# Optimization experiments

Measured on AMD Instinct MI355X. Metric: run time of the kernel, lower is better.

The kernel has to match this reference:

```python
import jax, jax.numpy as jnp
import numpy as np
from jax import lax

B, L = 2048, 2048
CIN, CONV, D, NCLS = 1, 128, 1024, 1000
E, H, K = 6, 2 * 1024, 2  # num_experts, expert hidden, top-k


def setup_inputs() -> dict:
    key = jax.random.key(0)
    ks = jax.random.split(key, 16)
    s = lambda *sh: 0.02
    return {
        "x": jax.random.normal(ks[0], (B, L), jnp.float32),
        "conv1_w": jax.random.normal(ks[1], (CONV, CIN, 5), jnp.float32) * 0.1,
        "conv1_b": jnp.zeros((CONV,), jnp.float32),
        "conv2_w": jax.random.normal(ks[2], (CONV, CONV, 5), jnp.float32) * 0.05,
        "conv2_b": jnp.zeros((CONV,), jnp.float32),
        "proj_w": jax.random.normal(ks[3], (D, CONV), jnp.float32) * 0.05,
        "proj_b": jnp.zeros((D,), jnp.float32),
        "router_w": jax.random.normal(ks[4], (E, D), jnp.float32) * 0.02,
        "router_b": jnp.zeros((E,), jnp.float32),
        "exp_w1": jax.random.normal(ks[5], (E, H, D), jnp.float32) * 0.02,
        "exp_b1": jnp.zeros((E, H), jnp.float32),
        "exp_w2": jax.random.normal(ks[6], (E, D, H), jnp.float32) * 0.02,
        "exp_b2": jnp.zeros((E, D), jnp.float32),
        "cls_w": jax.random.normal(ks[7], (NCLS, D), jnp.float32) * 0.02,
        "cls_b": jnp.zeros((NCLS,), jnp.float32),
    }


def _conv1d(x, w, b):
    # x: [B, C, L]; torch Conv1d(k=5, stride=2, pad=2)
    y = lax.conv_general_dilated(x, w, window_strides=(2,), padding=[(2, 2)],
                                 dimension_numbers=("NCH", "OIH", "NCH"))
    return y + b[None, :, None]


def reference(x, conv1_w, conv1_b, conv2_w, conv2_b, proj_w, proj_b,
              router_w, router_b, exp_w1, exp_b1, exp_w2, exp_b2, cls_w, cls_b):
    h = x[:, None, :]                               # [B,1,L]
    h = jax.nn.relu(_conv1d(h, conv1_w, conv1_b))   # [B,CONV,L/2]
    h = jax.nn.relu(_conv1d(h, conv2_w, conv2_b))   # [B,CONV,L/4]
    h = h.mean(axis=-1)                             # [B,CONV]
    h = h @ proj_w.T + proj_b                       # [B,D]

    # Top-2 router
    probs = jax.nn.softmax(h @ router_w.T + router_b, axis=-1)  # [B,E]
    top_vals, top_idx = lax.top_k(probs, K)                     # [B,2]
    # per-token per-expert combine weights (exact same math as masked loop)
    combine = (jax.nn.one_hot(top_idx[:, 0], E, dtype=h.dtype) * top_vals[:, 0:1]
               + jax.nn.one_hot(top_idx[:, 1], E, dtype=h.dtype) * top_vals[:, 1:2])  # [B,E]

    # all-expert FFN, then masked combine (equivalent to gather/scatter dispatch)
    hid = jax.nn.relu(jnp.einsum("bd,ehd->beh", h, exp_w1) + exp_b1)  # [B,E,H]
    eo = jnp.einsum("beh,edh->bed", hid, exp_w2) + exp_b2             # [B,E,D]
    moe = jnp.einsum("be,bed->bd", combine, eo)                       # [B,D]

    return moe @ cls_w.T + cls_b                                      # [B,NCLS]
```

## Files before the change

### kernel.cpp

```cpp
#include <hip/hip_runtime.h>
#include <hip/hip_bf16.h>
#include <hip/hip_fp16.h>
#include <stdint.h>

#define BB 2048
#define LL 2048
#define CV 128
#define DD 1024
#define NC 1000
#define EE 6
#define HH 2048

typedef __bf16 bf16_t;
typedef _Float16 f16_t;
typedef __attribute__((ext_vector_type(8))) __bf16 bf16x8;
typedef __attribute__((ext_vector_type(4))) __bf16 bf16x4;
typedef __attribute__((ext_vector_type(8))) _Float16 f16x8;
typedef __attribute__((ext_vector_type(4))) _Float16 f16x4;
typedef __attribute__((ext_vector_type(4))) float f32x4;

__global__ void k_prep_w2(const float* __restrict__ w2, bf16_t* __restrict__ wsw)
{
    int idx = blockIdx.x * 256 + threadIdx.x;
    if (idx >= 5 * 128 * 128) return;
    int kk = idx % 5;
    int t2 = idx / 5;
    int ci = t2 & 127;
    int co = t2 >> 7;
    float v = w2[idx];
    bf16_t h = (bf16_t)v;
    bf16_t l = (bf16_t)(v - (float)h);
    int t = (ci >> 5) * 5 + kk;
    int j = ci & 31;
    wsw[(size_t)t * 8192 + co * 32 + j]        = h;
    wsw[(size_t)t * 8192 + 4096 + co * 32 + j] = l;
}

__global__ void k_prep_exp(const float* __restrict__ ew1, const float* __restrict__ ew2,
                           const float* __restrict__ cw,  f16_t* __restrict__ ew1h,
                           f16_t* __restrict__ ew2h, f16_t* __restrict__ clsh)
{
    const size_t n1 = (size_t)EE * HH * DD / 4;
    const size_t n2 = n1 + (size_t)EE * DD * HH / 4;
    const size_t n3 = n2 + (size_t)NC * DD / 4;
    size_t i4 = (size_t)blockIdx.x * 256 + threadIdx.x;
    if (i4 >= n3) return;
    const float* src; f16_t* dst; size_t off;
    if (i4 < n1)      { src = ew1; dst = ew1h; off = i4; }
    else if (i4 < n2) { src = ew2; dst = ew2h; off = i4 - n1; }
    else              { src = cw;  dst = clsh; off = i4 - n2; }
    float4 v = reinterpret_cast<const float4*>(src)[off];
    f16x4 r;
    r[0] = (f16_t)v.x; r[1] = (f16_t)v.y; r[2] = (f16_t)v.z; r[3] = (f16_t)v.w;
    reinterpret_cast<f16x4*>(dst)[off] = r;
}

__launch_bounds__(256, 3)
__global__ void k_conv(const float* __restrict__ x,  const float* __restrict__ w1,
                       const float* __restrict__ b1, const bf16_t* __restrict__ wsw,
                       const float* __restrict__ b2, float* __restrict__ hbar)
{
    __shared__ __align__(16) float w1s[640];
    __shared__ __align__(16) float b1s[128];
    __shared__ __align__(16) float b2s[128];
    __shared__ __align__(16) float red[4][64];
    __shared__ __align__(16) float xs[528];
    __shared__ __align__(16) short h1s[2][8320];

    const int tid  = threadIdx.x;
    const int b    = blockIdx.x;
    const int lane = tid & 63;
    const int wid  = tid >> 6;
    const int l15  = lane & 15, lg = lane >> 4;
    const int wm   = wid >> 1,  wn = wid & 1;
    const int jo   = tid & 7;
    const int rg   = tid >> 3;

    for (int i = tid; i < 640; i += 256) w1s[i] = w1[i];
    if (tid < 128) { b1s[tid] = b1[tid]; b2s[tid] = b2[tid]; }

    const float* xrow = x + (size_t)b * LL;
    const int aoff = (wm * 64 + l15) * 32 + lg * 8;

    float racc[4][4];
#pragma unroll
    for (int m = 0; m < 4; ++m)
#pragma unroll
        for (int r = 0; r < 4; ++r) racc[m][r] = 0.f;

#define KSTEP(kk)                                                               \
    do {                                                                        \
        const bf16_t* wp_ = wsw + (size_t)(cb * 5 + (kk)) * 8192 + aoff;        \
        bf16x8 ah[4], al[4];                                                    \
        _Pragma("unroll")                                                       \
        for (int m = 0; m < 4; ++m) {                                           \
            ah[m] = *reinterpret_cast<const bf16x8*>(wp_ + m * 512);            \
            al[m] = *reinterpret_cast<const bf16x8*>(wp_ + 4096 + m * 512);     \
        }                                                                       \
        _Pragma("unroll")                                                       \
        for (int hf = 0; hf < 2; ++hf) {                                        \
            bf16x8 bh[2], bl[2];                                                \
            _Pragma("unroll")                                                   \
            for (int n2 = 0; n2 < 2; ++n2) {                                    \
                int r = 2 * (wn * 64 + (hf * 2 + n2) * 16 + l15) + (kk);        \
                int si = (r * 32 + lg * 8) ^ (((r >> 1) & 7) << 3);             \
                bh[n2] = *reinterpret_cast<const bf16x8*>(&h1s[0][si]);         \
                bl[n2] = *reinterpret_cast<const bf16x8*>(&h1s[1][si]);         \
            }                                                                   \
            _Pragma("unroll")                                                   \
            for (int m = 0; m < 4; ++m)                                         \
                _Pragma("unroll")                                               \
                for (int n2 = 0; n2 < 2; ++n2)                                  \
                    acc[m][hf * 2 + n2] = __builtin_amdgcn_mfma_f32_16x16x32_bf16(ah[m], bh[n2], acc[m][hf * 2 + n2], 0, 0, 0); \
            _Pragma("unroll")                                                   \
            for (int m = 0; m < 4; ++m)                                         \
                _Pragma("unroll")                                               \
                for (int n2 = 0; n2 < 2; ++n2)                                  \
                    acc[m][hf * 2 + n2] = __builtin_amdgcn_mfma_f32_16x16x32_bf16(ah[m], bl[n2], acc[m][hf * 2 + n2], 0, 0, 0); \
            _Pragma("unroll")                                                   \
            for (int m = 0; m < 4; ++m)                                         \
                _Pragma("unroll")                                               \
                for (int n2 = 0; n2 < 2; ++n2)                                  \
                    acc[m][hf * 2 + n2] = __builtin_amdgcn_mfma_f32_16x16x32_bf16(al[m], bh[n2], acc[m][hf * 2 + n2], 0, 0, 0); \
        }                                                                       \
    } while (0)

    for (int c = 0; c < 4; ++c) {
        const int t1base = 256 * c - 2;

        {
            const int xoff = 512 * c - 6;
            for (int i = tid; i < 528; i += 256) {
                int xg = xoff + i;
                xs[i] = ((unsigned)xg < 2048u) ? xrow[xg] : 0.f;
            }
        }

        f32x4 acc[4][4];
#pragma unroll
        for (int m = 0; m < 4; ++m)
#pragma unroll
            for (int n = 0; n < 4; ++n)
#pragma unroll
                for (int r = 0; r < 4; ++r) acc[m][n][r] = 0.f;

        for (int cb = 0; cb < 4; ++cb) {
            __syncthreads();

            const int ci0 = cb * 32 + jo * 4;
            float wf[20], br4[4];
#pragma unroll
            for (int q = 0; q < 5; ++q)
                *reinterpret_cast<float4*>(&wf[q * 4]) =
                    *reinterpret_cast<const float4*>(&w1s[ci0 * 5 + q * 4]);
            *reinterpret_cast<float4*>(&br4[0]) = *reinterpret_cast<const float4*>(&b1s[ci0]);

#pragma unroll 1
            for (int it = 0; it < 9; ++it) {
                int r = rg + it * 32;
                if (r < 260) {
                    bool valid = (unsigned)(t1base + r) < 1024u;
                    float xv[5];
#pragma unroll
                    for (int kk = 0; kk < 5; ++kk) xv[kk] = xs[2 * r + kk];
                    bf16x4 hv, lv;
#pragma unroll
                    for (int u = 0; u < 4; ++u) {
                        float v = br4[u];
#pragma unroll
                        for (int kk = 0; kk < 5; ++kk) v += wf[u * 5 + kk] * xv[kk];
                        v = valid ? fmaxf(v, 0.f) : 0.f;
                        bf16_t h = (bf16_t)v;
                        hv[u] = h;
                        lv[u] = (bf16_t)(v - (float)h);
                    }
                    int si = (r * 32 + jo * 4) ^ (((r >> 1) & 7) << 3);
                    *reinterpret_cast<bf16x4*>(&h1s[0][si]) = hv;
                    *reinterpret_cast<bf16x4*>(&h1s[1][si]) = lv;
                }
            }
            __syncthreads();

            KSTEP(0);
            KSTEP(1);
            KSTEP(2);
            KSTEP(3);
            KSTEP(4);
        }
#pragma unroll
        for (int m = 0; m < 4; ++m)
#pragma unroll
            for (int r = 0; r < 4; ++r) {
                int co = wm * 64 + m * 16 + lg * 4 + r;
                float bias = b2s[co];
                float s = 0.f;
#pragma unroll
                for (int n = 0; n < 4; ++n) s += fmaxf(acc[m][n][r] + bias, 0.f);
                racc[m][r] += s;
            }
    }
#undef KSTEP

#pragma unroll
    for (int m = 0; m < 4; ++m)
#pragma unroll
        for (int r = 0; r < 4; ++r) {
            float v = racc[m][r];
            v += __shfl_xor(v, 1);
            v += __shfl_xor(v, 2);
            v += __shfl_xor(v, 4);
            v += __shfl_xor(v, 8);
            racc[m][r] = v;
        }
    __syncthreads();
    if (l15 == 0) {
#pragma unroll
        for (int m = 0; m < 4; ++m)
#pragma unroll
            for (int r = 0; r < 4; ++r)
                red[wid][m * 16 + lg * 4 + r] = racc[m][r];
    }
    __syncthreads();
    if (tid < 128) {
        int wm2 = tid >> 6, loc = tid & 63;
        float s = red[wm2 * 2 + 0][loc] + red[wm2 * 2 + 1][loc];
        hbar[(size_t)b * 128 + tid] = s * (1.f / 512.f);
    }
}

__launch_bounds__(256)
__global__ void k_proj(const float* __restrict__ hbar, const float* __restrict__ pw,
                       const float* __restrict__ pb, float* __restrict__ h)
{
    __shared__ float hbs[64 * 128];
    const int tid = threadIdx.x;
    const int b0 = blockIdx.x * 64, d0 = blockIdx.y * 64;
    for (int i = tid * 4; i < 64 * 128; i += 1024)
        *reinterpret_cast<float4*>(&hbs[i]) =
            *reinterpret_cast<const float4*>(&hbar[(size_t)b0 * 128 + i]);
    __syncthreads();
    const int tx = tid & 15, ty = tid >> 4;
    float acc[4][4];
#pragma unroll
    for (int i = 0; i < 4; ++i)
#pragma unroll
        for (int j = 0; j < 4; ++j) acc[i][j] = 0.f;
    const float* pwr[4];
#pragma unroll
    for (int j = 0; j < 4; ++j) pwr[j] = pw + (size_t)(d0 + tx * 4 + j) * 128;
    for (int k = 0; k < 128; k += 4) {
        float4 wv[4], av[4];
#pragma unroll
        for (int j = 0; j < 4; ++j) wv[j] = *reinterpret_cast<const float4*>(pwr[j] + k);
#pragma unroll
        for (int i = 0; i < 4; ++i) av[i] = *reinterpret_cast<const float4*>(&hbs[(ty * 4 + i) * 128 + k]);
#pragma unroll
        for (int i = 0; i < 4; ++i)
#pragma unroll
            for (int j = 0; j < 4; ++j)
                acc[i][j] += av[i].x * wv[j].x + av[i].y * wv[j].y +
                             av[i].z * wv[j].z + av[i].w * wv[j].w;
    }
#pragma unroll
    for (int i = 0; i < 4; ++i) {
        int bb = b0 + ty * 4 + i;
#pragma unroll
        for (int j = 0; j < 4; ++j) {
            int d = d0 + tx * 4 + j;
            h[(size_t)bb * DD + d] = acc[i][j] + pb[d];
        }
    }
}

__launch_bounds__(256)
__global__ void k_router(const float* __restrict__ h, const float* __restrict__ rw,
                         const float* __restrict__ rb, float* __restrict__ comb,
                         int2* __restrict__ top)
{
    const int lane = threadIdx.x & 63;
    const int b = blockIdx.x * 4 + (threadIdx.x >> 6);
    float part[6] = {0.f, 0.f, 0.f, 0.f, 0.f, 0.f};
    for (int j = 0; j < 16; ++j) {
        int d = j * 64 + lane;
        float hv = h[(size_t)b * DD + d];
#pragma unroll
        for (int e = 0; e < 6; ++e) part[e] += rw[e * DD + d] * hv;
    }
#pragma unroll
    for (int e = 0; e < 6; ++e) {
        float v = part[e];
        for (int off = 32; off > 0; off >>= 1) v += __shfl_xor(v, off);
        part[e] = v;
    }
    if (lane == 0) {
        float lgt[6];
#pragma unroll
        for (int e = 0; e < 6; ++e) lgt[e] = part[e] + rb[e];
        int i1 = 0;
#pragma unroll
        for (int e = 1; e < 6; ++e) if (lgt[e] > lgt[i1]) i1 = e;
        int i2 = -1;
#pragma unroll
        for (int e = 0; e < 6; ++e)
            if (e != i1 && (i2 < 0 || lgt[e] > lgt[i2])) i2 = e;
        float mx = lgt[i1], s = 0.f, ex[6];
#pragma unroll
        for (int e = 0; e < 6; ++e) { ex[e] = expf(lgt[e] - mx); s += ex[e]; }
        float inv = 1.f / s;
#pragma unroll
        for (int e = 0; e < 6; ++e) comb[b * 8 + e] = 0.f;
        comb[b * 8 + 6] = 0.f; comb[b * 8 + 7] = 0.f;
        comb[b * 8 + i1] = ex[i1] * inv;
        comb[b * 8 + i2] = ex[i2] * inv;
        top[b] = make_int2(i1, i2);
    }
}

__global__ void k_index(const int2* __restrict__ top, int* __restrict__ meta,
                        int* __restrict__ idxg)
{
    __shared__ int wsum[4];
    const int tid = threadIdx.x, lane = tid & 63, wid = tid >> 6;
    int2 tk[8];
#pragma unroll
    for (int j = 0; j < 8; ++j) tk[j] = top[tid * 8 + j];
    int off_run = 0;
    for (int e = 0; e < 6; ++e) {
        int m[8], c = 0;
#pragma unroll
        for (int j = 0; j < 8; ++j) { m[j] = (tk[j].x == e || tk[j].y == e) ? 1 : 0; c += m[j]; }
        int v = c;
        for (int d = 1; d < 64; d <<= 1) { int u = __shfl_up(v, d); if (lane >= d) v += u; }
        if (lane == 63) wsum[wid] = v;
        __syncthreads();
        int wbase = 0;
#pragma unroll
        for (int w = 0; w < 4; ++w) if (w < wid) wbase += wsum[w];
        int total = wsum[0] + wsum[1] + wsum[2] + wsum[3];
        int p = off_run + wbase + (v - c);
#pragma unroll
        for (int j = 0; j < 8; ++j) if (m[j]) idxg[p++] = tid * 8 + j;
        if (tid == 0) { meta[e] = total; meta[8 + e] = off_run; }
        off_run += total;
        __syncthreads();
    }
    if (tid == 0) meta[14] = off_run;
}

__device__ inline f16x8 cvt8(const float4 a, const float4 b)
{
    f16x8 r;
    r[0] = (f16_t)a.x; r[1] = (f16_t)a.y; r[2] = (f16_t)a.z; r[3] = (f16_t)a.w;
    r[4] = (f16_t)b.x; r[5] = (f16_t)b.y; r[6] = (f16_t)b.z; r[7] = (f16_t)b.w;
    return r;
}

template<int EPI, int NFRAG>
__launch_bounds__(256, 3)
__global__ void k_moe(const float* __restrict__ hsrc, const f16_t* __restrict__ hidg,
                      const f16_t* __restrict__ eog, const float* __restrict__ Bp,
                      const f16_t* __restrict__ Bh, const float* __restrict__ bias,
                      f16_t* __restrict__ outH, f16_t* __restrict__ eogW,
                      float* __restrict__ outF, const float* __restrict__ comb,
                      const int2* __restrict__ top, const int* __restrict__ meta,
                      const int* __restrict__ idxg, int N, int K, int NCLIP)
{
    constexpr int BN = NFRAG * 32;
    __shared__ f16_t As[128 * 72];
    __shared__ f16_t Bs[BN * 72];
    const int tid = threadIdx.x;
    const int e  = blockIdx.z;
    const int m0 = blockIdx.x * 128, n0 = blockIdx.y * BN;
    int cnt = 1 << 30, off = 0;
    if (EPI != 3) {
        cnt = meta[e]; off = meta[8 + e];
        if (m0 >= cnt) return;
    }
    const int lane = tid & 63, wid = tid >> 6;
    const int l15 = lane & 15, lg = lane >> 4;
    const int wm = wid >> 1, wn = wid & 1;

    f32x4 acc[4][NFRAG];
#pragma unroll
    for (int i = 0; i < 4; ++i)
#pragma unroll
        for (int j = 0; j < NFRAG; ++j)
#pragma unroll
            for (int r = 0; r < 4; ++r) acc[i][j][r] = 0.f;

    for (int k0 = 0; k0 < K; k0 += 64) {
        __syncthreads();
        {
            const int row = tid >> 1, c0 = (tid & 1) * 32;
            f16x8* d = reinterpret_cast<f16x8*>(As + row * 72 + c0);
            if (EPI == 1) {
                int lr = m0 + row;
                int token = (lr < cnt) ? idxg[off + lr] : 0;
                const float4* s = reinterpret_cast<const float4*>(hsrc + (size_t)token * K + k0 + c0);
#pragma unroll
                for (int j = 0; j < 4; ++j) d[j] = cvt8(s[2 * j], s[2 * j + 1]);
            } else if (EPI == 2) {
                const uint4* s = reinterpret_cast<const uint4*>(hidg + (size_t)(off + m0 + row) * K + k0 + c0);
#pragma unroll
                for (int j = 0; j < 4; ++j) reinterpret_cast<uint4*>(d)[j] = s[j];
            } else {
                int r = m0 + row;
                const f16x8* s0 = reinterpret_cast<const f16x8*>(eog + ((size_t)r * 2) * K + k0 + c0);
                const f16x8* s1 = reinterpret_cast<const f16x8*>(eog + ((size_t)r * 2 + 1) * K + k0 + c0);
#pragma unroll
                for (int j = 0; j < 4; ++j) d[j] = s0[j] + s1[j];
            }
        }
        {
            constexpr int PERTHR = BN * 64 / 256;
            constexpr int TPR = 64 / PERTHR;
            const int row = tid / TPR, c0 = (tid % TPR) * PERTHR;
            const bool ok = (n0 + row) < NCLIP;
            f16x8* d = reinterpret_cast<f16x8*>(Bs + row * 72 + c0);
            if (Bh) {
                const uint4* s = reinterpret_cast<const uint4*>(
                    Bh + (size_t)e * N * K + (size_t)(n0 + row) * K + k0 + c0);
#pragma unroll
                for (int j = 0; j < PERTHR / 8; ++j) {
                    uint4 v = ok ? s[j] : make_uint4(0, 0, 0, 0);
                    reinterpret_cast<uint4*>(d)[j] = v;
                }
            } else {
                const float4* s = reinterpret_cast<const float4*>(
                    Bp + (size_t)e * N * K + (size_t)(n0 + row) * K + k0 + c0);
#pragma unroll
                for (int j = 0; j < PERTHR / 8; ++j) {
                    float4 a = ok ? s[2 * j]     : make_float4(0.f, 0.f, 0.f, 0.f);
                    float4 b = ok ? s[2 * j + 1] : make_float4(0.f, 0.f, 0.f, 0.f);
                    d[j] = cvt8(a, b);
                }
            }
        }
        __syncthreads();
#pragma unroll
        for (int kk = 0; kk < 64; kk += 32) {
            f16x8 af[4], bq[NFRAG];
#pragma unroll
            for (int i = 0; i < 4; ++i)
                af[i] = *reinterpret_cast<const f16x8*>(As + (wm * 64 + i * 16 + l15) * 72 + kk + lg * 8);
#pragma unroll
            for (int j = 0; j < NFRAG; ++j)
                bq[j] = *reinterpret_cast<const f16x8*>(Bs + (wn * (BN / 2) + j * 16 + l15) * 72 + kk + lg * 8);
#pragma unroll
            for (int i = 0; i < 4; ++i)
#pragma unroll
                for (int j = 0; j < NFRAG; ++j)
                    acc[i][j] = __builtin_amdgcn_mfma_f32_16x16x32_f16(af[i], bq[j], acc[i][j], 0, 0, 0);
        }
    }
#pragma unroll
    for (int i = 0; i < 4; ++i) {
#pragma unroll
        for (int j = 0; j < NFRAG; ++j) {
#pragma unroll
            for (int r = 0; r < 4; ++r) {
                int lr  = m0 + wm * 64 + i * 16 + lg * 4 + r;
                int col = n0 + wn * (BN / 2) + j * 16 + l15;
                float c = acc[i][j][r];
                if (EPI == 1) {
                    if (lr < cnt)
                        outH[(size_t)(off + lr) * N + col] = (f16_t)fmaxf(c + bias[(size_t)e * N + col], 0.f);
                } else if (EPI == 2) {
                    if (lr < cnt) {
                        int token = idxg[off + lr];
                        int slot = (top[token].x == e) ? 0 : 1;
                        float w = comb[token * 8 + e];
                        eogW[((size_t)token * 2 + slot) * N + col] = (f16_t)(w * (c + bias[(size_t)e * N + col]));
                    }
                } else {
                    if (col < NCLIP)
                        outF[(size_t)lr * NCLIP + col] = c + bias[col];
                }
            }
        }
    }
}

extern "C" void kernel_launch(void* const* d_in, const int* in_sizes, int n_in,
                              void* d_out, int out_size, void* d_ws, size_t ws_size,
                              hipStream_t stream)
{
    const float* x   = (const float*)d_in[0];
    const float* w1  = (const float*)d_in[1];
    const float* b1  = (const float*)d_in[2];
    const float* w2  = (const float*)d_in[3];
    const float* b2  = (const float*)d_in[4];
    const float* pw  = (const float*)d_in[5];
    const float* pb  = (const float*)d_in[6];
    const float* rw  = (const float*)d_in[7];
    const float* rb  = (const float*)d_in[8];
    const float* ew1 = (const float*)d_in[9];
    const float* eb1 = (const float*)d_in[10];
    const float* ew2 = (const float*)d_in[11];
    const float* eb2 = (const float*)d_in[12];
    const float* cw  = (const float*)d_in[13];
    const float* cb  = (const float*)d_in[14];
    float* out = (float*)d_out;

    char* ws = (char*)d_ws;
    bf16_t* wsw  = (bf16_t*)(ws + 0);
    float*  hbar = (float*)(ws + 327680);
    float*  h    = (float*)(ws + 1376256);
    f16_t*  eog  = (f16_t*)(ws + 1376256);
    float*  comb = (float*)(ws + 9764864);
    int2*   top  = (int2*)(ws + 9830400);
    int*    meta = (int*)(ws + 9846784);
    int*    idxg = (int*)(ws + 9847040);
    f16_t*  hidg = (f16_t*)(ws + 9863424);
    f16_t*  ew1h = (f16_t*)(ws + 27164928);
    f16_t*  ew2h = (f16_t*)(ws + 52330752);
    f16_t*  clsh = (f16_t*)(ws + 77496576);

    const bool f16w = ws_size >= 79593728ull;

    k_prep_w2<<<320, 256, 0, stream>>>(w2, wsw);
    if (f16w)
        k_prep_exp<<<25576, 256, 0, stream>>>(ew1, ew2, cw, ew1h, ew2h, clsh);
    k_conv<<<2048, 256, 0, stream>>>(x, w1, b1, wsw, b2, hbar);
    k_proj<<<dim3(32, 16), 256, 0, stream>>>(hbar, pw, pb, h);
    k_router<<<512, 256, 0, stream>>>(h, rw, rb, comb, top);
    k_index<<<1, 256, 0, stream>>>(top, meta, idxg);
    k_moe<1, 4><<<dim3(16, 16, 6), 256, 0, stream>>>(
        h, nullptr, nullptr, ew1, f16w ? ew1h : nullptr, eb1,
        hidg, nullptr, nullptr, comb, top, meta, idxg, HH, DD, HH);
    k_moe<2, 4><<<dim3(16, 8, 6), 256, 0, stream>>>(
        nullptr, hidg, nullptr, ew2, f16w ? ew2h : nullptr, eb2,
        nullptr, eog, nullptr, comb, top, meta, idxg, DD, HH, DD);
    k_moe<3, 2><<<dim3(16, 16, 1), 256, 0, stream>>>(
        nullptr, nullptr, eog, cw, f16w ? clsh : nullptr, cb,
        nullptr, nullptr, out, comb, top, meta, idxg, DD, DD, NC);
}
```

Measured before the change: 708.5 us.

## Software-pipeline conv1 production with conv2 MFMA via double-buffered LDS

Restructures the conv kernel into a 16-step pipeline. Each step computes the conv1 activations for the next channel block into a second LDS buffer, interleaved between the MFMA k-steps of the current block, and the x tile is also double-buffered. This cuts one barrier per step and lets VALU conv1 work overlap MFMA conv2 work. In exchange it doubles the h1 LDS footprint (about 66KB) and lowers the launch-bounds occupancy target from 3 to 2 blocks per CU.

```diff
diff --git a/kernel.cpp b/kernel.cpp
--- a/kernel.cpp
+++ b/kernel.cpp
@@ -55,7 +55,7 @@
     reinterpret_cast<f16x4*>(dst)[off] = r;
 }
 
-__launch_bounds__(256, 3)
+__launch_bounds__(256, 2)
 __global__ void k_conv(const float* __restrict__ x,  const float* __restrict__ w1,
                        const float* __restrict__ b1, const bf16_t* __restrict__ wsw,
                        const float* __restrict__ b2, float* __restrict__ hbar)
@@ -64,8 +64,8 @@
     __shared__ __align__(16) float b1s[128];
     __shared__ __align__(16) float b2s[128];
     __shared__ __align__(16) float red[4][64];
-    __shared__ __align__(16) float xs[528];
-    __shared__ __align__(16) short h1s[2][8320];
+    __shared__ __align__(16) float xsb[2][528];
+    __shared__ __align__(16) short h1s[2][2][8320];
 
     const int tid  = threadIdx.x;
     const int b    = blockIdx.x;
@@ -82,11 +82,50 @@
     const float* xrow = x + (size_t)b * LL;
     const int aoff = (wm * 64 + l15) * 32 + lg * 8;
 
+    for (int i = tid; i < 528; i += 256) {
+        int xg = -6 + i;
+        xsb[0][i] = ((unsigned)xg < 2048u) ? xrow[xg] : 0.f;
+    }
+    __syncthreads();
+
     float racc[4][4];
 #pragma unroll
     for (int m = 0; m < 4; ++m)
 #pragma unroll
         for (int r = 0; r < 4; ++r) racc[m][r] = 0.f;
+
+    f32x4 acc[4][4];
+#pragma unroll
+    for (int m = 0; m < 4; ++m)
+#pragma unroll
+        for (int n = 0; n < 4; ++n)
+#pragma unroll
+            for (int r = 0; r < 4; ++r) acc[m][n][r] = 0.f;
+
+#define C1IT(it)                                                                \
+    do {                                                                        \
+        int r_ = rg + (it) * 32;                                                \
+        if ((it) < 8 || r_ < 260) {                                             \
+            bool valid_ = (unsigned)(t1b_n + r_) < 1024u;                       \
+            float xv0 = xsp[2 * r_ + 0], xv1 = xsp[2 * r_ + 1];                 \
+            float xv2 = xsp[2 * r_ + 2], xv3 = xsp[2 * r_ + 3];                 \
+            float xv4 = xsp[2 * r_ + 4];                                        \
+            bf16x4 hv_, lv_;                                                    \
+            _Pragma("unroll")                                                   \
+            for (int u = 0; u < 4; ++u) {                                       \
+                float v_ = br4[u] + wf[u * 5 + 0] * xv0 + wf[u * 5 + 1] * xv1   \
+                         + wf[u * 5 + 2] * xv2 + wf[u * 5 + 3] * xv3            \
+                         + wf[u * 5 + 4] * xv4;                                 \
+                v_ = valid_ ? fmaxf(v_, 0.f) : 0.f;                             \
+                bf16_t h_ = (bf16_t)v_;                                         \
+                hv_[u] = h_;                                                    \
+                lv_[u] = (bf16_t)(v_ - (float)h_);                              \
+            }                                                                   \
+            int si_ = (r_ * 32 + jo * 4) ^ (((r_ >> 1) & 7) << 3);              \
+            *reinterpret_cast<bf16x4*>(h1nxt + si_) = hv_;                      \
+            *reinterpret_cast<bf16x4*>(h1nxt + 8320 + si_) = lv_;               \
+        }                                                                       \
+    } while (0)
 
 #define KSTEP(kk)                                                               \
     do {                                                                        \
@@ -102,10 +141,10 @@
             bf16x8 bh[2], bl[2];                                                \
             _Pragma("unroll")                                                   \
             for (int n2 = 0; n2 < 2; ++n2) {                                    \
-                int r = 2 * (wn * 64 + (hf * 2 + n2) * 16 + l15) + (kk);        \
-                int si = (r * 32 + lg * 8) ^ (((r >> 1) & 7) << 3);             \
-                bh[n2] = *reinterpret_cast<const bf16x8*>(&h1s[0][si]);         \
-                bl[n2] = *reinterpret_cast<const bf16x8*>(&h1s[1][si]);         \
+                int r_ = 2 * (wn * 64 + (hf * 2 + n2) * 16 + l15) + (kk);       \
+                int si_ = (r_ * 32 + lg * 8) ^ (((r_ >> 1) & 7) << 3);          \
+                bh[n2] = *reinterpret_cast<const bf16x8*>(h1cur + si_);         \
+                bl[n2] = *reinterpret_cast<const bf16x8*>(h1cur + 8320 + si_);  \
             }                                                                   \
             _Pragma("unroll")                                                   \
             for (int m = 0; m < 4; ++m)                                         \
@@ -125,81 +164,82 @@
         }                                                                       \
     } while (0)
 
-    for (int c = 0; c < 4; ++c) {
-        const int t1base = 256 * c - 2;
-
-        {
-            const int xoff = 512 * c - 6;
+    {
+        const float* xsp = xsb[0];
+        const int t1b_n = -2;
+        short* h1nxt = &h1s[0][0][0];
+        const int ci0 = jo * 4;
+        float wf[20], br4[4];
+#pragma unroll
+        for (int q = 0; q < 5; ++q)
+            *reinterpret_cast<float4*>(&wf[q * 4]) =
+                *reinterpret_cast<const float4*>(&w1s[ci0 * 5 + q * 4]);
+        *reinterpret_cast<float4*>(&br4[0]) = *reinterpret_cast<const float4*>(&b1s[ci0]);
+#pragma unroll 1
+        for (int it = 0; it < 9; ++it) {
+            C1IT(it);
+        }
+    }
+    __syncthreads();
+
+    for (int p = 0; p < 16; ++p) {
+        const int cb = p & 3;
+        const short* h1cur = &h1s[p & 1][0][0];
+
+        const int q = p + 1;
+        const bool do_c1 = (q < 16);
+        const int cn = q >> 2;
+        const int t1b_n = 256 * cn - 2;
+        const float* xsp = xsb[cn & 1];
+        short* h1nxt = &h1s[q & 1][0][0];
+        float wf[20], br4[4];
+        if (do_c1) {
+            const int ci0 = (q & 3) * 32 + jo * 4;
+#pragma unroll
+            for (int qq = 0; qq < 5; ++qq)
+                *reinterpret_cast<float4*>(&wf[qq * 4]) =
+                    *reinterpret_cast<const float4*>(&w1s[ci0 * 5 + qq * 4]);
+            *reinterpret_cast<float4*>(&br4[0]) = *reinterpret_cast<const float4*>(&b1s[ci0]);
+        }
+
+        KSTEP(0);
+        if (do_c1) { C1IT(0); C1IT(1); }
+        KSTEP(1);
+        if (do_c1) { C1IT(2); C1IT(3); }
+        KSTEP(2);
+        if (do_c1) { C1IT(4); C1IT(5); }
+        KSTEP(3);
+        if (do_c1) { C1IT(6); C1IT(7); }
+        KSTEP(4);
+        if (do_c1) { C1IT(8); }
+
+        if (((p + 2) & 3) == 0 && (p + 2) < 16) {
+            const int cs = (p + 2) >> 2;
             for (int i = tid; i < 528; i += 256) {
-                int xg = xoff + i;
-                xs[i] = ((unsigned)xg < 2048u) ? xrow[xg] : 0.f;
+                int xg = 512 * cs - 6 + i;
+                xsb[cs & 1][i] = ((unsigned)xg < 2048u) ? xrow[xg] : 0.f;
             }
         }
 
-        f32x4 acc[4][4];
-#pragma unroll
-        for (int m = 0; m < 4; ++m)
-#pragma unroll
-            for (int n = 0; n < 4; ++n)
-#pragma unroll
-                for (int r = 0; r < 4; ++r) acc[m][n][r] = 0.f;
-
-        for (int cb = 0; cb < 4; ++cb) {
-            __syncthreads();
-
-            const int ci0 = cb * 32 + jo * 4;
-            float wf[20], br4[4];
-#pragma unroll
-            for (int q = 0; q < 5; ++q)
-                *reinterpret_cast<float4*>(&wf[q * 4]) =
-                    *reinterpret_cast<const float4*>(&w1s[ci0 * 5 + q * 4]);
-            *reinterpret_cast<float4*>(&br4[0]) = *reinterpret_cast<const float4*>(&b1s[ci0]);
-
-#pragma unroll 1
-            for (int it = 0; it < 9; ++it) {
-                int r = rg + it * 32;
-                if (r < 260) {
-                    bool valid = (unsigned)(t1base + r) < 1024u;
-                    float xv[5];
-#pragma unroll
-                    for (int kk = 0; kk < 5; ++kk) xv[kk] = xs[2 * r + kk];
-                    bf16x4 hv, lv;
-#pragma unroll
-                    for (int u = 0; u < 4; ++u) {
-                        float v = br4[u];
-#pragma unroll
-                        for (int kk = 0; kk < 5; ++kk) v += wf[u * 5 + kk] * xv[kk];
-                        v = valid ? fmaxf(v, 0.f) : 0.f;
-                        bf16_t h = (bf16_t)v;
-                        hv[u] = h;
-                        lv[u] = (bf16_t)(v - (float)h);
-                    }
-                    int si = (r * 32 + jo * 4) ^ (((r >> 1) & 7) << 3);
-                    *reinterpret_cast<bf16x4*>(&h1s[0][si]) = hv;
-                    *reinterpret_cast<bf16x4*>(&h1s[1][si]) = lv;
+        if (cb == 3) {
+#pragma unroll
+            for (int m = 0; m < 4; ++m)
+#pragma unroll
+                for (int r = 0; r < 4; ++r) {
+                    int co = wm * 64 + m * 16 + lg * 4 + r;
+                    float bias = b2s[co];
+                    float s = 0.f;
+#pragma unroll
+                    for (int n = 0; n < 4; ++n) s += fmaxf(acc[m][n][r] + bias, 0.f);
+                    racc[m][r] += s;
+#pragma unroll
+                    for (int n = 0; n < 4; ++n) acc[m][n][r] = 0.f;
                 }
-            }
-            __syncthreads();
-
-            KSTEP(0);
-            KSTEP(1);
-            KSTEP(2);
-            KSTEP(3);
-            KSTEP(4);
-        }
-#pragma unroll
-        for (int m = 0; m < 4; ++m)
-#pragma unroll
-            for (int r = 0; r < 4; ++r) {
-                int co = wm * 64 + m * 16 + lg * 4 + r;
-                float bias = b2s[co];
-                float s = 0.f;
-#pragma unroll
-                for (int n = 0; n < 4; ++n) s += fmaxf(acc[m][n][r] + bias, 0.f);
-                racc[m][r] += s;
-            }
+        }
+        __syncthreads();
     }
 #undef KSTEP
+#undef C1IT
 
 #pragma unroll
     for (int m = 0; m < 4; ++m)
@@ -212,7 +252,6 @@
             v += __shfl_xor(v, 8);
             racc[m][r] = v;
         }
-    __syncthreads();
     if (l15 == 0) {
 #pragma unroll
         for (int m = 0; m < 4; ++m)
```

After: 814.1 us. 14.9% more time.
